# Kernel optimization log

Measured on AMD Instinct MI355X. Metric: run time of the kernel, lower is better.

Reference implementation:

```python
import jax, jax.numpy as jnp
import numpy as np

D_MODEL, D_K, C_DIM = 1024, 64, 64
B, S = 4, 4096


def setup_inputs() -> dict:
    key = jax.random.key(0)
    ks = jax.random.split(key, 10)
    sc = 1.0 / np.sqrt(D_MODEL)
    return {
        "X": jax.random.normal(ks[0], (B, S, D_MODEL), jnp.float32),
        "cultural_embedding": jax.random.normal(ks[1], (B, C_DIM), jnp.float32),
        "WQ": jax.random.normal(ks[2], (D_MODEL, D_K), jnp.float32) * sc,
        "bQ": jnp.zeros((D_K,), jnp.float32),
        "WK": jax.random.normal(ks[3], (D_MODEL, D_K), jnp.float32) * sc,
        "bK": jnp.zeros((D_K,), jnp.float32),
        "WV": jax.random.normal(ks[4], (D_MODEL, D_K), jnp.float32) * sc,
        "bV": jnp.zeros((D_K,), jnp.float32),
        "WC": jax.random.normal(ks[5], (C_DIM, D_K), jnp.float32) * (1.0 / np.sqrt(C_DIM)),
        "bC": jnp.zeros((D_K,), jnp.float32),
        "lam": jnp.float32(1.0),
    }


def reference(X, cultural_embedding, WQ, bQ, WK, bK, WV, bV, WC, bC, lam):
    # Projections: [B,S,d_k]
    Q = jnp.einsum('bsm,mk->bsk', X, WQ) + bQ
    K = jnp.einsum('bsm,mk->bsk', X, WK) + bK
    V = jnp.einsum('bsm,mk->bsk', X, WV) + bV
    # Cultural projection: [B,d_k]
    c_proj = cultural_embedding @ WC + bC
    # Base attention logits [B,S,S]
    base_logits = jnp.einsum('bqk,bsk->bqs', Q, K) / jnp.sqrt(jnp.float32(D_K))
    # Rank-1 cultural bias per query row, scalar lambda gate
    cultural_bias = lam * jnp.einsum('bsd,bd->bs', Q, c_proj)  # [B,S]
    combined = base_logits + cultural_bias[..., None]
    attn = jax.nn.softmax(combined, axis=-1)
    return jnp.einsum('bqs,bsk->bqk', attn, V)
```

## Files before the change

### kernel.cpp

```cpp
#include <hip/hip_runtime.h>

#define B_  4
#define S_  4096
#define DM  1024
#define DK  64
#define NSPLIT 8
#define KSPAN (S_ / NSPLIT)
#define QT  256

typedef _Float16 half8  __attribute__((ext_vector_type(8)));
typedef _Float16 half4v __attribute__((ext_vector_type(4)));
typedef __fp16   fp16x2 __attribute__((ext_vector_type(2)));
typedef float    floatx4 __attribute__((ext_vector_type(4)));

#define QSCALE 0.18033688011112042f
#define EXP2F(x) __builtin_amdgcn_exp2f(x)

__global__ __launch_bounds__(256) void wt_kernel(
    const float* __restrict__ WQ, const float* __restrict__ WK,
    const float* __restrict__ WV, _Float16* __restrict__ Wt)
{
    const int proj = blockIdx.y;
    const float* W = (proj == 0) ? WQ : (proj == 1) ? WK : WV;
    const int k0 = blockIdx.x * 64;
    const int t = threadIdx.x;
    __shared__ float T[64][68];

    #pragma unroll
    for (int p = 0; p < 4; p++) {
        int c = p * 256 + t;
        int k = c >> 4, n4 = (c & 15) * 4;
        float4 v = *(const float4*)(W + (size_t)(k0 + k) * DK + n4);
        T[k][n4 + 0] = v.x; T[k][n4 + 1] = v.y;
        T[k][n4 + 2] = v.z; T[k][n4 + 3] = v.w;
    }
    __syncthreads();

    const int n = t >> 2, kc = (t & 3) * 16;
    half8 h0, h1;
    #pragma unroll
    for (int j = 0; j < 8; j++) h0[j] = (_Float16)T[kc + j][n];
    #pragma unroll
    for (int j = 0; j < 8; j++) h1[j] = (_Float16)T[kc + 8 + j][n];
    _Float16* dst = Wt + ((size_t)proj * 64 + n) * DM + k0 + kc;
    *(half8*)(dst)     = h0;
    *(half8*)(dst + 8) = h1;
}

__global__ __launch_bounds__(256) void proj_mfma_kernel(
    const float* __restrict__ X, const _Float16* __restrict__ Wt,
    const float* __restrict__ bQ, const float* __restrict__ bK,
    const float* __restrict__ bV,
    _Float16* __restrict__ Qh, _Float16* __restrict__ Kh,
    _Float16* __restrict__ Vt)
{
    const int r0   = blockIdx.x * 64;
    const int t    = threadIdx.x;
    const int wave = t >> 6, lane = t & 63;
    const int quad = lane >> 4, l15 = lane & 15;

    __shared__ __align__(16) _Float16 Xs[64 * 72];
    __shared__ __align__(16) _Float16 Ws[3][64 * 72];

    floatx4 acc[3][4];
    #pragma unroll
    for (int p = 0; p < 3; p++)
        #pragma unroll
        for (int nt = 0; nt < 4; nt++)
            acc[p][nt] = (floatx4){0.f, 0.f, 0.f, 0.f};

    int xrow[4], xcol[4];
    #pragma unroll
    for (int p = 0; p < 4; p++) {
        int c = p * 256 + t;
        xrow[p] = c >> 4; xcol[p] = (c & 15) * 4;
    }
    int wrow[2], wcol[2];
    #pragma unroll
    for (int p = 0; p < 2; p++) {
        int c = p * 256 + t;
        wrow[p] = c >> 3; wcol[p] = (c & 7) * 8;
    }

    float4 xr[4]; half8 wr[3][2];
    #pragma unroll
    for (int p = 0; p < 4; p++)
        xr[p] = *(const float4*)(X + (size_t)(r0 + xrow[p]) * DM + xcol[p]);
    #pragma unroll
    for (int pr = 0; pr < 3; pr++)
        #pragma unroll
        for (int p = 0; p < 2; p++)
            wr[pr][p] = *(const half8*)(Wt + ((size_t)pr * 64 + wrow[p]) * DM + wcol[p]);

    for (int kt = 0; kt < DM / 64; kt++) {
        __syncthreads();
        #pragma unroll
        for (int p = 0; p < 4; p++) {
            half4v h;
            h[0] = (_Float16)xr[p].x; h[1] = (_Float16)xr[p].y;
            h[2] = (_Float16)xr[p].z; h[3] = (_Float16)xr[p].w;
            *(half4v*)&Xs[xrow[p] * 72 + xcol[p]] = h;
        }
        #pragma unroll
        for (int pr = 0; pr < 3; pr++)
            #pragma unroll
            for (int p = 0; p < 2; p++)
                *(half8*)&Ws[pr][wrow[p] * 72 + wcol[p]] = wr[pr][p];
        __syncthreads();

        if (kt + 1 < DM / 64) {
            const int kn = (kt + 1) * 64;
            #pragma unroll
            for (int p = 0; p < 4; p++)
                xr[p] = *(const float4*)(X + (size_t)(r0 + xrow[p]) * DM + kn + xcol[p]);
            #pragma unroll
            for (int pr = 0; pr < 3; pr++)
                #pragma unroll
                for (int p = 0; p < 2; p++)
                    wr[pr][p] = *(const half8*)(Wt + ((size_t)pr * 64 + wrow[p]) * DM + kn + wcol[p]);
        }

        half8 xa0 = *(half8*)&Xs[(wave * 16 + l15) * 72 + quad * 8];
        half8 xa1 = *(half8*)&Xs[(wave * 16 + l15) * 72 + 32 + quad * 8];
        #pragma unroll
        for (int pr = 0; pr < 3; pr++) {
            #pragma unroll
            for (int nt = 0; nt < 4; nt++) {
                half8 bf0 = *(half8*)&Ws[pr][(nt * 16 + l15) * 72 + quad * 8];
                half8 bf1 = *(half8*)&Ws[pr][(nt * 16 + l15) * 72 + 32 + quad * 8];
                floatx4 a = acc[pr][nt];
                a = __builtin_amdgcn_mfma_f32_16x16x32_f16(xa0, bf0, a, 0, 0, 0);
                a = __builtin_amdgcn_mfma_f32_16x16x32_f16(xa1, bf1, a, 0, 0, 0);
                acc[pr][nt] = a;
            }
        }
    }

    float bqv[4], bkv[4], bvv[4];
    #pragma unroll
    for (int nt = 0; nt < 4; nt++) {
        bqv[nt] = bQ[nt * 16 + l15];
        bkv[nt] = bK[nt * 16 + l15];
        bvv[nt] = bV[nt * 16 + l15];
    }

    const int orow = r0 + wave * 16 + quad * 4;
    const int bidx = r0 >> 12;
    const int s0   = (r0 & (S_ - 1)) + wave * 16 + quad * 4;
    #pragma unroll
    for (int nt = 0; nt < 4; nt++) {
        const int d = nt * 16 + l15;
        #pragma unroll
        for (int i = 0; i < 4; i++) {
            Qh[(size_t)(orow + i) * DK + d] =
                (_Float16)((acc[0][nt][i] + bqv[nt]) * QSCALE);
            Kh[(size_t)(orow + i) * DK + d] =
                (_Float16)(acc[1][nt][i] + bkv[nt]);
        }
        half4v hv;
        #pragma unroll
        for (int i = 0; i < 4; i++)
            hv[i] = (_Float16)(acc[2][nt][i] + bvv[nt]);
        *(half4v*)(Vt + (size_t)bidx * DK * S_ + (size_t)d * S_ + s0) = hv;
    }
}

__global__ __launch_bounds__(512, 4) void flash_mfma_kernel(
    const _Float16* __restrict__ Qh, const _Float16* __restrict__ Kh,
    const _Float16* __restrict__ Vt, _Float16* __restrict__ Oph,
    float* __restrict__ Lp)
{
    const int b     = blockIdx.y;
    const int q0    = blockIdx.x * QT;
    const int split = blockIdx.z;
    const int kbase = split * KSPAN;
    const int t     = threadIdx.x;
    const int wave  = t >> 6, lane = t & 63;
    const int quad  = lane >> 4, l15 = lane & 15;

    __shared__ __align__(16) _Float16 Ks[2][64 * 72];
    __shared__ __align__(16) _Float16 Vs[2][64 * 72];

    const _Float16* Qb = Qh + ((size_t)b * S_ + q0) * DK;
    const _Float16* Kb = Kh + ((size_t)b * S_ + kbase) * DK;
    const _Float16* Vb = Vt + (size_t)b * DK * S_ + kbase;

    half8 qf0[2], qf1[2];
    #pragma unroll
    for (int mt = 0; mt < 2; mt++) {
        const _Float16* qr = Qb + (size_t)(wave * 32 + mt * 16 + l15) * DK;
        qf0[mt] = *(const half8*)(qr + quad * 8);
        qf1[mt] = *(const half8*)(qr + 32 + quad * 8);
    }

    floatx4 acc[2][4];
    float rs[2];
    #pragma unroll
    for (int mt = 0; mt < 2; mt++) {
        #pragma unroll
        for (int nt = 0; nt < 4; nt++) acc[mt][nt] = (floatx4){0.f,0.f,0.f,0.f};
        rs[mt] = 0.f;
    }

    const int kr   = t >> 3, kcol = (t & 7) * 8;
    const int krP  = (kr & 32) | ((kr & 4) << 2) | ((kr & 24) >> 1) | (kr & 3);
    half8 kreg = *(const half8*)(Kb + (size_t)kr * DK + kcol);
    half8 vreg = *(const half8*)(Vb + (size_t)kr * S_ + kcol);
    *(half8*)&Ks[0][krP * 72 + kcol] = kreg;
    *(half8*)&Vs[0][kr  * 72 + kcol] = vreg;

    const int NT = KSPAN / 64;
    int cur = 0;
    for (int it = 0; it < NT; it++) {
        __syncthreads();

        if (it + 1 < NT) {
            const int kn = (it + 1) * 64;
            kreg = *(const half8*)(Kb + (size_t)(kn + kr) * DK + kcol);
            vreg = *(const half8*)(Vb + (size_t)kr * S_ + kn + kcol);
        }

        floatx4 sc[2][4];
        __builtin_amdgcn_s_setprio(1);
        #pragma unroll
        for (int nt = 0; nt < 4; nt++) {
            half8 kf0 = *(half8*)&Ks[cur][(nt * 16 + l15) * 72 + quad * 8];
            half8 kf1 = *(half8*)&Ks[cur][(nt * 16 + l15) * 72 + 32 + quad * 8];
            #pragma unroll
            for (int mt = 0; mt < 2; mt++) {
                floatx4 z = (floatx4){0.f, 0.f, 0.f, 0.f};
                z = __builtin_amdgcn_mfma_f32_16x16x32_f16(kf0, qf0[mt], z, 0, 0, 0);
                z = __builtin_amdgcn_mfma_f32_16x16x32_f16(kf1, qf1[mt], z, 0, 0, 0);
                sc[mt][nt] = z;
            }
        }
        __builtin_amdgcn_s_setprio(0);

        half8 pf0[2], pf1[2];
        #pragma unroll
        for (int mt = 0; mt < 2; mt++) {
            float pe[4][4];
            #pragma unroll
            for (int nt = 0; nt < 4; nt++)
                #pragma unroll
                for (int i = 0; i < 4; i++) {
                    pe[nt][i] = EXP2F(sc[mt][nt][i]);
                    rs[mt] += pe[nt][i];
                }
            fp16x2 c0 = __builtin_amdgcn_cvt_pkrtz(pe[0][0], pe[0][1]);
            fp16x2 c1 = __builtin_amdgcn_cvt_pkrtz(pe[0][2], pe[0][3]);
            fp16x2 c2 = __builtin_amdgcn_cvt_pkrtz(pe[1][0], pe[1][1]);
            fp16x2 c3 = __builtin_amdgcn_cvt_pkrtz(pe[1][2], pe[1][3]);
            pf0[mt] = (half8){(_Float16)c0[0], (_Float16)c0[1],
                              (_Float16)c1[0], (_Float16)c1[1],
                              (_Float16)c2[0], (_Float16)c2[1],
                              (_Float16)c3[0], (_Float16)c3[1]};
            fp16x2 c4 = __builtin_amdgcn_cvt_pkrtz(pe[2][0], pe[2][1]);
            fp16x2 c5 = __builtin_amdgcn_cvt_pkrtz(pe[2][2], pe[2][3]);
            fp16x2 c6 = __builtin_amdgcn_cvt_pkrtz(pe[3][0], pe[3][1]);
            fp16x2 c7 = __builtin_amdgcn_cvt_pkrtz(pe[3][2], pe[3][3]);
            pf1[mt] = (half8){(_Float16)c4[0], (_Float16)c4[1],
                              (_Float16)c5[0], (_Float16)c5[1],
                              (_Float16)c6[0], (_Float16)c6[1],
                              (_Float16)c7[0], (_Float16)c7[1]};
        }

        __builtin_amdgcn_s_setprio(1);
        #pragma unroll
        for (int nt = 0; nt < 4; nt++) {
            half8 vf0 = *(half8*)&Vs[cur][(nt * 16 + l15) * 72 + quad * 8];
            half8 vf1 = *(half8*)&Vs[cur][(nt * 16 + l15) * 72 + 32 + quad * 8];
            #pragma unroll
            for (int mt = 0; mt < 2; mt++) {
                floatx4 a = acc[mt][nt];
                a = __builtin_amdgcn_mfma_f32_16x16x32_f16(vf0, pf0[mt], a, 0, 0, 0);
                a = __builtin_amdgcn_mfma_f32_16x16x32_f16(vf1, pf1[mt], a, 0, 0, 0);
                acc[mt][nt] = a;
            }
        }
        __builtin_amdgcn_s_setprio(0);

        if (it + 1 < NT) {
            *(half8*)&Ks[cur ^ 1][krP * 72 + kcol] = kreg;
            *(half8*)&Vs[cur ^ 1][kr  * 72 + kcol] = vreg;
        }
        cur ^= 1;
    }

    const size_t prow = (size_t)split * B_ * S_ + (size_t)b * S_ + q0;
    #pragma unroll
    for (int mt = 0; mt < 2; mt++) {
        float r = rs[mt];
        r += __shfl_xor(r, 16, 64);
        r += __shfl_xor(r, 32, 64);
        const float inv = 1.0f / r;
        const size_t orow = prow + wave * 32 + mt * 16 + l15;
        #pragma unroll
        for (int nt = 0; nt < 4; nt++) {
            half4v hv;
            #pragma unroll
            for (int i = 0; i < 4; i++)
                hv[i] = (_Float16)(acc[mt][nt][i] * inv);
            *(half4v*)(Oph + orow * DK + nt * 16 + quad * 4) = hv;
        }
        if (quad == 0)
            Lp[orow] = r;
    }
}

__global__ __launch_bounds__(256) void combine_kernel(
    const _Float16* __restrict__ Oph, const float* __restrict__ Lp,
    float* __restrict__ O)
{
    const int r  = blockIdx.x * 16 + (threadIdx.x >> 4);
    const int d4 = (threadIdx.x & 15) * 4;
    const int NR = B_ * S_;

    float lw[NSPLIT], lsum = 0.f;
    #pragma unroll
    for (int s = 0; s < NSPLIT; s++) {
        lw[s] = Lp[(size_t)s * NR + r];
        lsum += lw[s];
    }
    const float inv = 1.0f / lsum;

    float o[4] = {0.f, 0.f, 0.f, 0.f};
    #pragma unroll
    for (int s = 0; s < NSPLIT; s++) {
        half4v h = *(const half4v*)(Oph + ((size_t)s * NR + r) * DK + d4);
        const float w = lw[s];
        #pragma unroll
        for (int j = 0; j < 4; j++) o[j] += w * (float)h[j];
    }
    float4 out;
    out.x = o[0] * inv; out.y = o[1] * inv;
    out.z = o[2] * inv; out.w = o[3] * inv;
    *(float4*)(O + (size_t)r * DK + d4) = out;
}

extern "C" void kernel_launch(void* const* d_in, const int* in_sizes, int n_in,
                              void* d_out, int out_size, void* d_ws, size_t ws_size,
                              hipStream_t stream)
{
    const float* X  = (const float*)d_in[0];
    const float* WQ = (const float*)d_in[2];
    const float* bQ = (const float*)d_in[3];
    const float* WK = (const float*)d_in[4];
    const float* bK = (const float*)d_in[5];
    const float* WV = (const float*)d_in[6];
    const float* bV = (const float*)d_in[7];

    char* ws = (char*)d_ws;
    _Float16* Qh  = (_Float16*)ws;  ws += (size_t)B_ * S_ * DK * 2;
    _Float16* Kh  = (_Float16*)ws;  ws += (size_t)B_ * S_ * DK * 2;
    _Float16* Vt  = (_Float16*)ws;  ws += (size_t)B_ * S_ * DK * 2;
    _Float16* Wt  = (_Float16*)ws;  ws += (size_t)3 * 64 * DM * 2;
    _Float16* Oph = (_Float16*)ws;  ws += (size_t)NSPLIT * B_ * S_ * DK * 2;
    float* Lp     = (float*)ws;

    wt_kernel<<<dim3(DM / 64, 3), 256, 0, stream>>>(WQ, WK, WV, Wt);

    proj_mfma_kernel<<<dim3((B_ * S_) / 64), 256, 0, stream>>>(
        X, Wt, bQ, bK, bV, Qh, Kh, Vt);

    flash_mfma_kernel<<<dim3(S_ / QT, B_, NSPLIT), 512, 0, stream>>>(
        Qh, Kh, Vt, Oph, Lp);

    combine_kernel<<<dim3((B_ * S_) / 16), 256, 0, stream>>>(
        Oph, Lp, (float*)d_out);
}
```

Before: 151.8 us.

## Load projection operands directly from global into MFMA fragments, dropping LDS staging

The projection kernel no longer stages X and W tiles through shared memory with two barriers per k-step. Each lane instead loads its own X fragment from global memory, converts it to fp16 in registers, and reads W fragments straight from global memory. A two-tile-deep register prefetch and a fully unrolled k loop hide load latency. The trade-off is that W fragments are now read by every wave instead of shared through LDS, which raises global/L2 traffic and register pressure.

Result: slower. 189.0 us (+24.5%).

```diff
diff --git a/kernel.cpp b/kernel.cpp
--- a/kernel.cpp
+++ b/kernel.cpp
@@ -47,6 +47,16 @@
     *(half8*)(dst + 8) = h1;
 }
 
+__device__ inline half8 cvt8_rte(float4 a, float4 b)
+{
+    half8 h;
+    h[0] = (_Float16)a.x; h[1] = (_Float16)a.y;
+    h[2] = (_Float16)a.z; h[3] = (_Float16)a.w;
+    h[4] = (_Float16)b.x; h[5] = (_Float16)b.y;
+    h[6] = (_Float16)b.z; h[7] = (_Float16)b.w;
+    return h;
+}
+
 __global__ __launch_bounds__(256) void proj_mfma_kernel(
     const float* __restrict__ X, const _Float16* __restrict__ Wt,
     const float* __restrict__ bQ, const float* __restrict__ bK,
@@ -59,8 +69,7 @@
     const int wave = t >> 6, lane = t & 63;
     const int quad = lane >> 4, l15 = lane & 15;
 
-    __shared__ __align__(16) _Float16 Xs[64 * 72];
-    __shared__ __align__(16) _Float16 Ws[3][64 * 72];
+    const float* xrow = X + (size_t)(r0 + wave * 16 + l15) * DM;
 
     floatx4 acc[3][4];
     #pragma unroll
@@ -69,72 +78,45 @@
         for (int nt = 0; nt < 4; nt++)
             acc[p][nt] = (floatx4){0.f, 0.f, 0.f, 0.f};
 
-    int xrow[4], xcol[4];
-    #pragma unroll
-    for (int p = 0; p < 4; p++) {
-        int c = p * 256 + t;
-        xrow[p] = c >> 4; xcol[p] = (c & 15) * 4;
-    }
-    int wrow[2], wcol[2];
-    #pragma unroll
-    for (int p = 0; p < 2; p++) {
-        int c = p * 256 + t;
-        wrow[p] = c >> 3; wcol[p] = (c & 7) * 8;
-    }
-
-    float4 xr[4]; half8 wr[3][2];
-    #pragma unroll
-    for (int p = 0; p < 4; p++)
-        xr[p] = *(const float4*)(X + (size_t)(r0 + xrow[p]) * DM + xcol[p]);
-    #pragma unroll
-    for (int pr = 0; pr < 3; pr++)
-        #pragma unroll
-        for (int p = 0; p < 2; p++)
-            wr[pr][p] = *(const half8*)(Wt + ((size_t)pr * 64 + wrow[p]) * DM + wcol[p]);
-
+#define LOADX(dst, k)                                                   \
+    {                                                                   \
+        const float* p_ = xrow + (k) * 64 + quad * 8;                   \
+        dst[0] = *(const float4*)(p_);                                  \
+        dst[1] = *(const float4*)(p_ + 4);                              \
+        dst[2] = *(const float4*)(p_ + 32);                             \
+        dst[3] = *(const float4*)(p_ + 36);                             \
+    }
+
+    float4 xA[4], xB[4], xC[4];
+    LOADX(xA, 0);
+    LOADX(xB, 1);
+
+    #pragma unroll
     for (int kt = 0; kt < DM / 64; kt++) {
-        __syncthreads();
-        #pragma unroll
-        for (int p = 0; p < 4; p++) {
-            half4v h;
-            h[0] = (_Float16)xr[p].x; h[1] = (_Float16)xr[p].y;
-            h[2] = (_Float16)xr[p].z; h[3] = (_Float16)xr[p].w;
-            *(half4v*)&Xs[xrow[p] * 72 + xcol[p]] = h;
-        }
-        #pragma unroll
-        for (int pr = 0; pr < 3; pr++)
-            #pragma unroll
-            for (int p = 0; p < 2; p++)
-                *(half8*)&Ws[pr][wrow[p] * 72 + wcol[p]] = wr[pr][p];
-        __syncthreads();
-
-        if (kt + 1 < DM / 64) {
-            const int kn = (kt + 1) * 64;
-            #pragma unroll
-            for (int p = 0; p < 4; p++)
-                xr[p] = *(const float4*)(X + (size_t)(r0 + xrow[p]) * DM + kn + xcol[p]);
-            #pragma unroll
-            for (int pr = 0; pr < 3; pr++)
-                #pragma unroll
-                for (int p = 0; p < 2; p++)
-                    wr[pr][p] = *(const half8*)(Wt + ((size_t)pr * 64 + wrow[p]) * DM + kn + wcol[p]);
-        }
-
-        half8 xa0 = *(half8*)&Xs[(wave * 16 + l15) * 72 + quad * 8];
-        half8 xa1 = *(half8*)&Xs[(wave * 16 + l15) * 72 + 32 + quad * 8];
+        if (kt + 2 < DM / 64) LOADX(xC, kt + 2);
+
+        half8 xa0 = cvt8_rte(xA[0], xA[1]);
+        half8 xa1 = cvt8_rte(xA[2], xA[3]);
+
         #pragma unroll
         for (int pr = 0; pr < 3; pr++) {
             #pragma unroll
             for (int nt = 0; nt < 4; nt++) {
-                half8 bf0 = *(half8*)&Ws[pr][(nt * 16 + l15) * 72 + quad * 8];
-                half8 bf1 = *(half8*)&Ws[pr][(nt * 16 + l15) * 72 + 32 + quad * 8];
+                const _Float16* wp =
+                    Wt + ((size_t)pr * 64 + nt * 16 + l15) * DM + kt * 64 + quad * 8;
+                half8 bf0 = *(const half8*)(wp);
+                half8 bf1 = *(const half8*)(wp + 32);
                 floatx4 a = acc[pr][nt];
                 a = __builtin_amdgcn_mfma_f32_16x16x32_f16(xa0, bf0, a, 0, 0, 0);
                 a = __builtin_amdgcn_mfma_f32_16x16x32_f16(xa1, bf1, a, 0, 0, 0);
                 acc[pr][nt] = a;
             }
         }
-    }
+
+        #pragma unroll
+        for (int j = 0; j < 4; j++) { xA[j] = xB[j]; xB[j] = xC[j]; }
+    }
+#undef LOADX
 
     float bqv[4], bkv[4], bvv[4];
     #pragma unroll
```
